# Kernel optimization log

Measured on AMD Instinct MI355X. Metric: run time of the kernel, lower is better.

Reference implementation:

```python
import jax, jax.numpy as jnp
import numpy as np


def setup_inputs() -> dict:
    key = jax.random.key(0)
    k1, k2, k3, k4 = jax.random.split(key, 4)
    B, C, H, W = 8, 256, 64, 64
    x = jax.random.normal(k1, (B, C, H, W), dtype=jnp.float32)
    wq = jax.random.normal(k2, (1, C), dtype=jnp.float32) * (1.0 / np.sqrt(C))
    wk = jax.random.normal(k3, (1, C), dtype=jnp.float32) * (1.0 / np.sqrt(C))
    wv = jax.random.normal(k4, (C, C), dtype=jnp.float32) * (1.0 / np.sqrt(C))
    gamma = jnp.zeros((1,), dtype=jnp.float32)
    return {"x": x, "wq": wq, "wk": wk, "wv": wv, "gamma": gamma}


def reference(x, wq, wk, wv, gamma):
    B, C, H, W = x.shape
    N = H * W
    xf = x.reshape(B, C, N)                      # [B, C, N]
    # 1x1 convs == channel matmuls
    f = jnp.einsum('oc,bcn->bon', wq, xf)        # [B, 1, N]
    g = jnp.einsum('oc,bcn->bon', wk, xf)        # [B, 1, N]
    h = jnp.einsum('oc,bcn->bon', wv, xf)        # [B, C, N]
    # scores[b, i, j] = f[b, 0, i] * g[b, 0, j]  -> [B, N, N]
    scores = jnp.einsum('bi,bj->bij', f[:, 0, :], g[:, 0, :])
    # softmax over dim=1 (rows), matching torch F.softmax(..., dim=1)
    beta = jax.nn.softmax(scores, axis=1)        # [B, N, N]
    gam = gamma[0]
    o = (1.0 - gam) * jnp.einsum('bcn,bnm->bcm', h, beta) + gam * xf
    return o.reshape(B, C, H, W)
```

## Files before the change

### kernel.cpp

```cpp
#include <hip/hip_runtime.h>
#include <math.h>

#define BQ 8
#define CQ 256
#define NQ 4096
#define MT 64
#define NSUP 64

typedef short s16x8 __attribute__((ext_vector_type(8)));
typedef short s16x4 __attribute__((ext_vector_type(4)));
typedef float f32x4 __attribute__((ext_vector_type(4)));
typedef unsigned int uint;

static __device__ __forceinline__ float4 ld4(const float* p) { return *(const float4*)p; }

static constexpr float LOG2E = 1.4426950408889634f;

static __device__ __forceinline__ short f2bf(float f) {
    return __builtin_bit_cast(short, (__bf16)f);
}
static __device__ __forceinline__ uint fkey(float f) {
    uint b = __builtin_bit_cast(uint, f);
    return b ^ (0x80000000u | (uint)((int)b >> 31));
}
static __device__ __forceinline__ float fdec(uint u) {
    uint b = (u & 0x80000000u) ? (u ^ 0x80000000u) : ~u;
    return __builtin_bit_cast(float, b);
}

__global__ void k_fg(const float* __restrict__ x, const float* __restrict__ wq,
                     const float* __restrict__ wk, float* __restrict__ fs,
                     float* __restrict__ g, short* __restrict__ xbf,
                     uint* __restrict__ fmxu, uint* __restrict__ fmnu) {
    int b = blockIdx.y;
    int t = threadIdx.x;
    int nl = (t & 31) * 2;
    int cg = t >> 5;
    int n = blockIdx.x * 64 + nl;
    const float* xb = x + (size_t)b * CQ * NQ + n;
    uint* xo = (uint*)(xbf + (size_t)b * CQ * NQ + n);
    float f0 = 0.f, f1 = 0.f, g0 = 0.f, g1 = 0.f;
    int c0 = cg * 32;
#pragma unroll 8
    for (int c = c0; c < c0 + 32; ++c) {
        float2 v = *(const float2*)&xb[(size_t)c * NQ];
        f0 = fmaf(wq[c], v.x, f0);
        f1 = fmaf(wq[c], v.y, f1);
        g0 = fmaf(wk[c], v.x, g0);
        g1 = fmaf(wk[c], v.y, g1);
        uint p = (uint)(unsigned short)f2bf(v.x) | ((uint)(unsigned short)f2bf(v.y) << 16);
        xo[c * (NQ / 2)] = p;
    }
    __shared__ float sf[8][64], sg2[8][64];
    sf[cg][nl] = f0;  sf[cg][nl + 1] = f1;
    sg2[cg][nl] = g0; sg2[cg][nl + 1] = g1;
    __syncthreads();
    if (t < 64) {
        float f = 0.f, gg = 0.f;
#pragma unroll
        for (int i = 0; i < 8; ++i) { f += sf[i][t]; gg += sg2[i][t]; }
        f *= LOG2E;
        fs[b * NQ + blockIdx.x * 64 + t] = f;
        g[b * NQ + blockIdx.x * 64 + t]  = gg;
        float mx = f, mn = f;
#pragma unroll
        for (int off = 32; off; off >>= 1) {
            mx = fmaxf(mx, __shfl_xor(mx, off));
            mn = fminf(mn, __shfl_xor(mn, off));
        }
        if (t == 0) {
            atomicMax(&fmxu[b], fkey(mx));
            atomicMin(&fmnu[b], fkey(mn));
        }
    }
}

#define ZBUF_OFF 65536
#define SMEM_BYTES 66560

__global__ void __launch_bounds__(512, 4) k_attn(
    const short* __restrict__ xbf, const float* __restrict__ fsp,
    const float* __restrict__ gp, const uint* __restrict__ fmxu,
    const uint* __restrict__ fmnu, const float* __restrict__ wv,
    const float* __restrict__ x, const float* __restrict__ gamma,
    float* __restrict__ out) {
    __shared__ __align__(16) char smem[SMEM_BYTES];

    int bid = blockIdx.x;
    int b = bid & 7;
    int mblk = bid >> 3;
    int m0 = mblk * MT;
    int tid = threadIdx.x;
    int l = tid & 63;
    int w = tid >> 6;
    int ws = w & 1;
    int wm = (w >> 1) & 1;
    int wc = w >> 2;
    int q = l >> 4;
    int cr = l & 15;
    int qp16 = (q ^ ((cr >> 1) & 3)) * 16;

    const short* xb = xbf + (size_t)b * CQ * NQ;
    const float* fb = fsp + b * NQ;

    const short* srcs[4];
    int dsts[4];
#pragma unroll
    for (int r2 = 0; r2 < 4; ++r2) {
        int row = (tid >> 2) + (r2 & 1) * 128;
        int half = r2 >> 1;
        int lq = (tid & 3) ^ ((row >> 1) & 3);
        srcs[r2] = xb + (size_t)row * NQ + half * 32 + lq * 8;
        dsts[r2] = tid * 16 + r2 * 8192;
    }

#pragma unroll
    for (int r2 = 0; r2 < 4; ++r2) {
        __builtin_amdgcn_global_load_lds(
            (const __attribute__((address_space(1))) void*)srcs[r2],
            (__attribute__((address_space(3))) void*)(smem + dsts[r2]), 16, 0, 0);
        srcs[r2] += 64;
    }

    float fmx = fdec(fmxu[b]), fmn = fdec(fmnu[b]);
    const float* gb = gp + b * NQ;
    float gj[2], nM[2];
#pragma unroll
    for (int jm = 0; jm < 2; ++jm) {
        float gv = gb[m0 + wm * 32 + jm * 16 + cr];
        gj[jm] = gv;
        nM[jm] = -((gv >= 0.f) ? gv * fmx : gv * fmn);
    }

    s16x8 ones;
#pragma unroll
    for (int i = 0; i < 8; ++i) ones[i] = (short)0x3F80;

    f32x4 acc[8][2];
#pragma unroll
    for (int jc = 0; jc < 8; ++jc)
#pragma unroll
        for (int jm = 0; jm < 2; ++jm) acc[jc][jm] = (f32x4){0.f, 0.f, 0.f, 0.f};
    f32x4 accz[2] = {(f32x4){0.f, 0.f, 0.f, 0.f}, (f32x4){0.f, 0.f, 0.f, 0.f}};

    __syncthreads();

    for (int s = 0; s < NSUP; ++s) {
        if (s < NSUP - 1) {
            char* nbuf = smem + ((s + 1) & 1) * 32768;
#pragma unroll
            for (int r2 = 0; r2 < 4; ++r2) {
                __builtin_amdgcn_global_load_lds(
                    (const __attribute__((address_space(1))) void*)srcs[r2],
                    (__attribute__((address_space(3))) void*)(nbuf + dsts[r2]), 16, 0, 0);
                srcs[r2] += 64;
            }
        }
        int chunk = 2 * s + ws;
        const char* cbuf = smem + (s & 1) * 32768 + ws * 16384;
        const float* fls = fb + chunk * 32;
        float4 fqa = ld4(fls + q * 8);
        float4 fqb = ld4(fls + q * 8 + 4);
        float fq[8] = {fqa.x, fqa.y, fqa.z, fqa.w, fqb.x, fqb.y, fqb.z, fqb.w};
        s16x8 bv[2];
#pragma unroll
        for (int jm = 0; jm < 2; ++jm) {
#pragma unroll
            for (int i = 0; i < 8; ++i)
                bv[jm][i] = f2bf(__builtin_amdgcn_exp2f(fmaf(fq[i], gj[jm], nM[jm])));
        }
        accz[0] = __builtin_amdgcn_mfma_f32_16x16x32_bf16(ones, bv[0], accz[0], 0, 0, 0);
        accz[1] = __builtin_amdgcn_mfma_f32_16x16x32_bf16(ones, bv[1], accz[1], 0, 0, 0);
#pragma unroll
        for (int jc = 0; jc < 8; ++jc) {
            s16x8 av = *(const s16x8*)(cbuf + (wc * 128 + jc * 16 + cr) * 64 + qp16);
            acc[jc][0] = __builtin_amdgcn_mfma_f32_16x16x32_bf16(av, bv[0], acc[jc][0], 0, 0, 0);
            acc[jc][1] = __builtin_amdgcn_mfma_f32_16x16x32_bf16(av, bv[1], acc[jc][1], 0, 0, 0);
        }
        __syncthreads();
    }

    float zf[2] = {accz[0][0], accz[1][0]};
    float* zb = (float*)(smem + ZBUF_OFF);
    if (q == 0) {
#pragma unroll
        for (int jm = 0; jm < 2; ++jm) zb[w * 32 + jm * 16 + cr] = zf[jm];
    }
    __syncthreads();
#pragma unroll
    for (int jm = 0; jm < 2; ++jm) zf[jm] += zb[(w ^ 1) * 32 + jm * 16 + cr];

    {
        int p = wc * 2 + wm;
        float* mrg = (float*)(smem + p * 16384);
        if (ws == 1) {
#pragma unroll
            for (int jc = 0; jc < 8; ++jc)
#pragma unroll
                for (int jm = 0; jm < 2; ++jm)
                    *(f32x4*)(mrg + ((jc * 2 + jm) * 64 + l) * 4) = acc[jc][jm];
        }
        __syncthreads();
        if (ws == 0) {
#pragma unroll
            for (int jc = 0; jc < 8; ++jc)
#pragma unroll
                for (int jm = 0; jm < 2; ++jm) {
                    f32x4 o = *(const f32x4*)(mrg + ((jc * 2 + jm) * 64 + l) * 4);
                    acc[jc][jm] += o;
                }
        }
        __syncthreads();
    }

    if (ws == 0) {
        float rzl[2];
#pragma unroll
        for (int jm = 0; jm < 2; ++jm) rzl[jm] = 1.0f / zf[jm];
#pragma unroll
        for (int jc = 0; jc < 8; ++jc) {
#pragma unroll
            for (int jm = 0; jm < 2; ++jm) {
                int mloc = wm * 32 + jm * 16 + cr;
                int cb = (wc * 256 + jc * 32 + q * 8) ^ ((mloc & 7) << 4);
                s16x4 v;
#pragma unroll
                for (int r = 0; r < 4; ++r) v[r] = f2bf(acc[jc][jm][r] * rzl[jm]);
                *(s16x4*)(smem + mloc * 512 + cb) = v;
            }
        }
    }
    __syncthreads();

    int co0 = w * 32;
    f32x4 acc2[2][4];
#pragma unroll
    for (int j2 = 0; j2 < 2; ++j2)
#pragma unroll
        for (int jm2 = 0; jm2 < 4; ++jm2) acc2[j2][jm2] = (f32x4){0.f, 0.f, 0.f, 0.f};

#pragma unroll 2
    for (int ks = 0; ks < 8; ++ks) {
        s16x8 a2[2];
#pragma unroll
        for (int j2 = 0; j2 < 2; ++j2) {
            const float* wr = wv + (size_t)(co0 + j2 * 16 + cr) * CQ + ks * 32 + q * 8;
            float4 wa = ld4(wr);
            float4 wb = ld4(wr + 4);
            a2[j2][0] = f2bf(wa.x); a2[j2][1] = f2bf(wa.y);
            a2[j2][2] = f2bf(wa.z); a2[j2][3] = f2bf(wa.w);
            a2[j2][4] = f2bf(wb.x); a2[j2][5] = f2bf(wb.y);
            a2[j2][6] = f2bf(wb.z); a2[j2][7] = f2bf(wb.w);
        }
#pragma unroll
        for (int jm2 = 0; jm2 < 4; ++jm2) {
            int mloc = jm2 * 16 + cr;
            s16x8 b2 = *(const s16x8*)(smem + mloc * 512 + ((ks * 64 + q * 16) ^ ((mloc & 7) << 4)));
#pragma unroll
            for (int j2 = 0; j2 < 2; ++j2)
                acc2[j2][jm2] = __builtin_amdgcn_mfma_f32_16x16x32_bf16(a2[j2], b2, acc2[j2][jm2], 0, 0, 0);
        }
    }

    float gam = gamma[0];
    float omg = 1.f - gam;
    if (gam != 0.f) {
#pragma unroll
        for (int j2 = 0; j2 < 2; ++j2)
#pragma unroll
            for (int jm2 = 0; jm2 < 4; ++jm2)
#pragma unroll
                for (int r = 0; r < 4; ++r) {
                    int c_out = co0 + j2 * 16 + q * 4 + r;
                    size_t idx = ((size_t)b * CQ + c_out) * NQ + m0 + jm2 * 16 + cr;
                    __builtin_nontemporal_store(
                        fmaf(gam, x[idx], acc2[j2][jm2][r] * omg), out + idx);
                }
    } else {
#pragma unroll
        for (int j2 = 0; j2 < 2; ++j2)
#pragma unroll
            for (int jm2 = 0; jm2 < 4; ++jm2)
#pragma unroll
                for (int r = 0; r < 4; ++r) {
                    int c_out = co0 + j2 * 16 + q * 4 + r;
                    size_t idx = ((size_t)b * CQ + c_out) * NQ + m0 + jm2 * 16 + cr;
                    __builtin_nontemporal_store(acc2[j2][jm2][r] * omg, out + idx);
                }
    }
}

extern "C" void kernel_launch(void* const* d_in, const int* in_sizes, int n_in,
                              void* d_out, int out_size, void* d_ws, size_t ws_size,
                              hipStream_t stream) {
    const float* x     = (const float*)d_in[0];
    const float* wq    = (const float*)d_in[1];
    const float* wk    = (const float*)d_in[2];
    const float* wv    = (const float*)d_in[3];
    const float* gamma = (const float*)d_in[4];
    float* out = (float*)d_out;

    float* ws  = (float*)d_ws;
    float* fs  = ws;
    float* g   = ws + BQ * NQ;
    uint* fmxu = (uint*)(ws + 2 * BQ * NQ);
    uint* fmnu = fmxu + 8;
    short* xbf = (short*)(ws + 2 * BQ * NQ + 64);

    hipMemsetAsync(fmxu, 0x00, 32, stream);
    hipMemsetAsync(fmnu, 0xFF, 32, stream);
    hipLaunchKernelGGL(k_fg, dim3(NQ / 64, BQ), dim3(256), 0, stream,
                       x, wq, wk, fs, g, xbf, fmxu, fmnu);
    hipLaunchKernelGGL(k_attn, dim3(BQ * (NQ / MT)), dim3(512), 0, stream,
                       xbf, fs, g, fmxu, fmnu, wv, x, gamma, out);
}
```

Baseline: 129.2 us.

## Specialize warps into exp producers and MFMA consumers with LDS handoff

Splits the 8 waves into 4 producer waves that compute the exp weights (and row sums) one chunk ahead into a double-buffered LDS slot, and 4 consumer waves that run the bf16 MFMAs over 128 smaller 32-wide chunks. The old design had every wave compute exp redundantly and split K across wave pairs, followed by a cross-wave merge of accumulators. The new layout removes that redundant exp work, the ones-MFMA normalizer, and the merge step, and it shrinks shared memory. In exchange, only half the waves issue MFMAs, there are twice as many block-wide barriers, and the swizzled LDS layout is gone, so bank conflicts may increase.

```diff
diff --git a/kernel.cpp b/kernel.cpp
--- a/kernel.cpp
+++ b/kernel.cpp
@@ -5,7 +5,7 @@
 #define CQ 256
 #define NQ 4096
 #define MT 64
-#define NSUP 64
+#define NCH 128
 
 typedef short s16x8 __attribute__((ext_vector_type(8)));
 typedef short s16x4 __attribute__((ext_vector_type(4)));
@@ -75,8 +75,24 @@
     }
 }
 
-#define ZBUF_OFF 65536
-#define SMEM_BYTES 66560
+#define EOFF 32768
+#define ESLOT 5120
+#define ZOFF 43008
+#define SMEM_BYTES 44032
+
+#define STAGE(slot, ch)                                                            \
+    {                                                                              \
+        _Pragma("unroll")                                                          \
+        for (int i_ = 0; i_ < 2; ++i_) {                                           \
+            int off_ = tid * 16 + i_ * 8192;                                       \
+            int row_ = off_ >> 6, nb_ = off_ & 63;                                 \
+            const short* src_ = xb + (size_t)row_ * NQ + (ch) * 32 + (nb_ >> 1);   \
+            __builtin_amdgcn_global_load_lds(                                      \
+                (const __attribute__((address_space(1))) void*)src_,               \
+                (__attribute__((address_space(3))) void*)(smem + (slot) * 16384 + off_), \
+                16, 0, 0);                                                         \
+        }                                                                          \
+    }
 
 __global__ void __launch_bounds__(512, 4) k_attn(
     const short* __restrict__ xbf, const float* __restrict__ fsp,
@@ -93,130 +109,89 @@
     int tid = threadIdx.x;
     int l = tid & 63;
     int w = tid >> 6;
-    int ws = w & 1;
-    int wm = (w >> 1) & 1;
-    int wc = w >> 2;
     int q = l >> 4;
     int cr = l & 15;
-    int qp16 = (q ^ ((cr >> 1) & 3)) * 16;
 
     const short* xb = xbf + (size_t)b * CQ * NQ;
     const float* fb = fsp + b * NQ;
 
-    const short* srcs[4];
-    int dsts[4];
-#pragma unroll
-    for (int r2 = 0; r2 < 4; ++r2) {
-        int row = (tid >> 2) + (r2 & 1) * 128;
-        int half = r2 >> 1;
-        int lq = (tid & 3) ^ ((row >> 1) & 3);
-        srcs[r2] = xb + (size_t)row * NQ + half * 32 + lq * 8;
-        dsts[r2] = tid * 16 + r2 * 8192;
-    }
-
-#pragma unroll
-    for (int r2 = 0; r2 < 4; ++r2) {
-        __builtin_amdgcn_global_load_lds(
-            (const __attribute__((address_space(1))) void*)srcs[r2],
-            (__attribute__((address_space(3))) void*)(smem + dsts[r2]), 16, 0, 0);
-        srcs[r2] += 64;
-    }
-
-    float fmx = fdec(fmxu[b]), fmn = fdec(fmnu[b]);
-    const float* gb = gp + b * NQ;
-    float gj[2], nM[2];
-#pragma unroll
-    for (int jm = 0; jm < 2; ++jm) {
-        float gv = gb[m0 + wm * 32 + jm * 16 + cr];
-        gj[jm] = gv;
-        nM[jm] = -((gv >= 0.f) ? gv * fmx : gv * fmn);
-    }
-
-    s16x8 ones;
-#pragma unroll
-    for (int i = 0; i < 8; ++i) ones[i] = (short)0x3F80;
-
+    STAGE(0, 0)
+
+    int wc = w >> 1;
+    int wm = w & 1;
     f32x4 acc[8][2];
 #pragma unroll
     for (int jc = 0; jc < 8; ++jc)
 #pragma unroll
         for (int jm = 0; jm < 2; ++jm) acc[jc][jm] = (f32x4){0.f, 0.f, 0.f, 0.f};
-    f32x4 accz[2] = {(f32x4){0.f, 0.f, 0.f, 0.f}, (f32x4){0.f, 0.f, 0.f, 0.f}};
-
-    __syncthreads();
-
-    for (int s = 0; s < NSUP; ++s) {
-        if (s < NSUP - 1) {
-            char* nbuf = smem + ((s + 1) & 1) * 32768;
-#pragma unroll
-            for (int r2 = 0; r2 < 4; ++r2) {
-                __builtin_amdgcn_global_load_lds(
-                    (const __attribute__((address_space(1))) void*)srcs[r2],
-                    (__attribute__((address_space(3))) void*)(nbuf + dsts[r2]), 16, 0, 0);
-                srcs[r2] += 64;
+
+    int p = w - 4;
+    float gv = 0.f, nM = 0.f, zac = 0.f;
+    float4 fca = {0,0,0,0}, fcb = {0,0,0,0}, fna = {0,0,0,0}, fnb = {0,0,0,0};
+
+    if (w >= 4) {
+        float fmx = fdec(fmxu[b]), fmn = fdec(fmnu[b]);
+        gv = gp[b * NQ + m0 + l];
+        nM = -((gv >= 0.f) ? gv * fmx : gv * fmn);
+        float4 a0 = ld4(fb + p * 8);
+        float4 b0 = ld4(fb + p * 8 + 4);
+        float fq[8] = {a0.x, a0.y, a0.z, a0.w, b0.x, b0.y, b0.z, b0.w};
+        s16x8 ev;
+#pragma unroll
+        for (int i = 0; i < 8; ++i) {
+            float e = __builtin_amdgcn_exp2f(fmaf(fq[i], gv, nM));
+            zac += e;
+            ev[i] = f2bf(e);
+        }
+        *(s16x8*)(smem + EOFF + l * 80 + p * 16) = ev;
+        fca = ld4(fb + 32 + p * 8);  fcb = ld4(fb + 32 + p * 8 + 4);
+        fna = ld4(fb + 64 + p * 8);  fnb = ld4(fb + 64 + p * 8 + 4);
+    }
+    __syncthreads();
+
+    for (int s = 0; s < NCH; ++s) {
+        if (s + 1 < NCH) STAGE((s + 1) & 1, s + 1)
+        if (w < 4) {
+            const char* cbuf = smem + (s & 1) * 16384;
+            const char* ebuf = smem + EOFF + (s & 1) * ESLOT;
+            s16x8 bv0 = *(const s16x8*)(ebuf + (wm * 32 + cr) * 80 + q * 16);
+            s16x8 bv1 = *(const s16x8*)(ebuf + (wm * 32 + 16 + cr) * 80 + q * 16);
+#pragma unroll
+            for (int jc = 0; jc < 8; ++jc) {
+                s16x8 av = *(const s16x8*)(cbuf + (wc * 128 + jc * 16 + cr) * 64 + q * 16);
+                acc[jc][0] = __builtin_amdgcn_mfma_f32_16x16x32_bf16(av, bv0, acc[jc][0], 0, 0, 0);
+                acc[jc][1] = __builtin_amdgcn_mfma_f32_16x16x32_bf16(av, bv1, acc[jc][1], 0, 0, 0);
             }
-        }
-        int chunk = 2 * s + ws;
-        const char* cbuf = smem + (s & 1) * 32768 + ws * 16384;
-        const float* fls = fb + chunk * 32;
-        float4 fqa = ld4(fls + q * 8);
-        float4 fqb = ld4(fls + q * 8 + 4);
-        float fq[8] = {fqa.x, fqa.y, fqa.z, fqa.w, fqb.x, fqb.y, fqb.z, fqb.w};
-        s16x8 bv[2];
+        } else if (s + 1 < NCH) {
+            float fq[8] = {fca.x, fca.y, fca.z, fca.w, fcb.x, fcb.y, fcb.z, fcb.w};
+            s16x8 ev;
+#pragma unroll
+            for (int i = 0; i < 8; ++i) {
+                float e = __builtin_amdgcn_exp2f(fmaf(fq[i], gv, nM));
+                zac += e;
+                ev[i] = f2bf(e);
+            }
+            *(s16x8*)(smem + EOFF + ((s + 1) & 1) * ESLOT + l * 80 + p * 16) = ev;
+            fca = fna; fcb = fnb;
+            int ch = (s + 3) & (NCH - 1);
+            fna = ld4(fb + ch * 32 + p * 8);
+            fnb = ld4(fb + ch * 32 + p * 8 + 4);
+        }
+        __syncthreads();
+    }
+
+    if (w >= 4) ((float*)(smem + ZOFF))[p * 64 + l] = zac;
+    __syncthreads();
+
+    if (w < 4) {
+        const float* zb = (const float*)(smem + ZOFF);
+        float rzl[2];
 #pragma unroll
         for (int jm = 0; jm < 2; ++jm) {
-#pragma unroll
-            for (int i = 0; i < 8; ++i)
-                bv[jm][i] = f2bf(__builtin_amdgcn_exp2f(fmaf(fq[i], gj[jm], nM[jm])));
-        }
-        accz[0] = __builtin_amdgcn_mfma_f32_16x16x32_bf16(ones, bv[0], accz[0], 0, 0, 0);
-        accz[1] = __builtin_amdgcn_mfma_f32_16x16x32_bf16(ones, bv[1], accz[1], 0, 0, 0);
-#pragma unroll
-        for (int jc = 0; jc < 8; ++jc) {
-            s16x8 av = *(const s16x8*)(cbuf + (wc * 128 + jc * 16 + cr) * 64 + qp16);
-            acc[jc][0] = __builtin_amdgcn_mfma_f32_16x16x32_bf16(av, bv[0], acc[jc][0], 0, 0, 0);
-            acc[jc][1] = __builtin_amdgcn_mfma_f32_16x16x32_bf16(av, bv[1], acc[jc][1], 0, 0, 0);
-        }
-        __syncthreads();
-    }
-
-    float zf[2] = {accz[0][0], accz[1][0]};
-    float* zb = (float*)(smem + ZBUF_OFF);
-    if (q == 0) {
-#pragma unroll
-        for (int jm = 0; jm < 2; ++jm) zb[w * 32 + jm * 16 + cr] = zf[jm];
-    }
-    __syncthreads();
-#pragma unroll
-    for (int jm = 0; jm < 2; ++jm) zf[jm] += zb[(w ^ 1) * 32 + jm * 16 + cr];
-
-    {
-        int p = wc * 2 + wm;
-        float* mrg = (float*)(smem + p * 16384);
-        if (ws == 1) {
-#pragma unroll
-            for (int jc = 0; jc < 8; ++jc)
-#pragma unroll
-                for (int jm = 0; jm < 2; ++jm)
-                    *(f32x4*)(mrg + ((jc * 2 + jm) * 64 + l) * 4) = acc[jc][jm];
-        }
-        __syncthreads();
-        if (ws == 0) {
-#pragma unroll
-            for (int jc = 0; jc < 8; ++jc)
-#pragma unroll
-                for (int jm = 0; jm < 2; ++jm) {
-                    f32x4 o = *(const f32x4*)(mrg + ((jc * 2 + jm) * 64 + l) * 4);
-                    acc[jc][jm] += o;
-                }
-        }
-        __syncthreads();
-    }
-
-    if (ws == 0) {
-        float rzl[2];
-#pragma unroll
-        for (int jm = 0; jm < 2; ++jm) rzl[jm] = 1.0f / zf[jm];
+            int mloc = wm * 32 + jm * 16 + cr;
+            float z = zb[mloc] + zb[64 + mloc] + zb[128 + mloc] + zb[192 + mloc];
+            rzl[jm] = 1.0f / z;
+        }
 #pragma unroll
         for (int jc = 0; jc < 8; ++jc) {
 #pragma unroll
```

Result: slower. 137.4 us (+6.3%).
